# Optimization experiments

Hardware: AMD Instinct MI355X
Metric: run time of the kernel (lower is better)

The kernel has to match this reference:

```python
import jax, jax.numpy as jnp
import numpy as np

B, T, C, H = 4, 2048, 768, 12
D = C // H
EPS = 1e-5


def layernorm(x, g, b):
    mu = jnp.mean(x, axis=-1, keepdims=True)
    var = jnp.mean(jnp.square(x - mu), axis=-1, keepdims=True)
    return (x - mu) * jax.lax.rsqrt(var + EPS) * g + b


def setup_inputs() -> dict:
    key = jax.random.key(0)
    ks = jax.random.split(key, 16)
    s = 0.02
    return {
        "x": jax.random.normal(ks[0], (B, T, C), jnp.float32),
        "Wq": jax.random.normal(ks[1], (C, C), jnp.float32) * s,
        "bq": jnp.zeros((C,), jnp.float32),
        "Wk": jax.random.normal(ks[2], (C, C), jnp.float32) * s,
        "bk": jnp.zeros((C,), jnp.float32),
        "Wv": jax.random.normal(ks[3], (C, C), jnp.float32) * s,
        "bv": jnp.zeros((C,), jnp.float32),
        "Wo": jax.random.normal(ks[4], (C, C), jnp.float32) * s,
        "bo": jnp.zeros((C,), jnp.float32),
        "g1": jnp.ones((C,), jnp.float32),
        "b1": jnp.zeros((C,), jnp.float32),
        "g2": jnp.ones((C,), jnp.float32),
        "b2": jnp.zeros((C,), jnp.float32),
        "W1": jax.random.normal(ks[5], (C, 4 * C), jnp.float32) * s,
        "bm1": jnp.zeros((4 * C,), jnp.float32),
        "W2": jax.random.normal(ks[6], (4 * C, C), jnp.float32) * s,
        "bm2": jnp.zeros((C,), jnp.float32),
    }


def reference(x, Wq, bq, Wk, bk, Wv, bv, Wo, bo, g1, b1, g2, b2, W1, bm1, W2, bm2):
    # --- attention branch ---
    h = layernorm(x, g1, b1)
    q = (h @ Wq + bq).reshape(B, T, H, D)
    k = (h @ Wk + bk).reshape(B, T, H, D)
    v = (h @ Wv + bv).reshape(B, T, H, D)
    att = jnp.einsum('bqhd,bkhd->bhqk', q, k) / jnp.sqrt(jnp.float32(D))
    causal = jnp.tril(jnp.ones((T, T), bool))
    att = jnp.where(causal, att, -jnp.inf)
    att = jax.nn.softmax(att, axis=-1)
    o = jnp.einsum('bhqk,bkhd->bqhd', att, v).reshape(B, T, C)
    x = x + o @ Wo + bo
    # --- MLP branch ---
    h = layernorm(x, g2, b2)
    h = jax.nn.gelu(h @ W1 + bm1, approximate=False)
    return x + h @ W2 + bm2
```

## Files before the change

kernel.cpp:

```cpp
#include <hip/hip_runtime.h>
#include <hip/hip_bf16.h>

#define B_ 4
#define T_ 2048
#define C_ 768
#define H_ 12
#define D_ 64
#define QS_ 2304

typedef __attribute__((ext_vector_type(8))) short short8;
typedef __attribute__((ext_vector_type(4))) short short4v;
typedef __attribute__((ext_vector_type(4))) float f32x4;

__device__ __forceinline__ unsigned short f2bf(float f) {
    __hip_bfloat16 h = __float2bfloat16(f);
    return *reinterpret_cast<unsigned short*>(&h);
}

__device__ __forceinline__ unsigned cvt_pk_bf16(float lo, float hi) {
    unsigned r;
    asm("v_cvt_pk_bf16_f32 %0, %1, %2" : "=v"(r) : "v"(lo), "v"(hi));
    return r;
}

__device__ __forceinline__ void gl_lds16(const void* g, void* l) {
    __builtin_amdgcn_global_load_lds((const __attribute__((address_space(1))) unsigned int*)g,
                                     (__attribute__((address_space(3))) unsigned int*)l,
                                     16, 0, 0);
}

__global__ __launch_bounds__(256) void ln_f32_bf16(const float* __restrict__ x,
                                                   const float* __restrict__ g,
                                                   const float* __restrict__ b,
                                                   unsigned short* __restrict__ out) {
    int row = blockIdx.x;
    int tid = threadIdx.x;
    const float* xr = x + (size_t)row * C_;
    float v0 = xr[tid], v1 = xr[tid + 256], v2 = xr[tid + 512];
    float s = v0 + v1 + v2;
    #pragma unroll
    for (int off = 1; off < 64; off <<= 1) s += __shfl_xor(s, off);
    __shared__ float ws1[4], ws2[4];
    int wid = tid >> 6, lane = tid & 63;
    if (lane == 0) ws1[wid] = s;
    __syncthreads();
    float mean = (ws1[0] + ws1[1] + ws1[2] + ws1[3]) * (1.0f / C_);
    float d0 = v0 - mean, d1 = v1 - mean, d2 = v2 - mean;
    float qs = d0*d0 + d1*d1 + d2*d2;
    #pragma unroll
    for (int off = 1; off < 64; off <<= 1) qs += __shfl_xor(qs, off);
    if (lane == 0) ws2[wid] = qs;
    __syncthreads();
    float var = (ws2[0] + ws2[1] + ws2[2] + ws2[3]) * (1.0f / C_);
    float rs = rsqrtf(var + 1e-5f);
    unsigned short* orow = out + (size_t)row * C_;
    orow[tid]       = f2bf(d0 * rs * g[tid]       + b[tid]);
    orow[tid + 256] = f2bf(d1 * rs * g[tid + 256] + b[tid + 256]);
    orow[tid + 512] = f2bf(d2 * rs * g[tid + 512] + b[tid + 512]);
}

__global__ __launch_bounds__(256) void transpose_bf16(const float* __restrict__ W,
                                                      unsigned short* __restrict__ Wt,
                                                      int K, int N) {
    __shared__ float t[64][65];
    int n0 = blockIdx.x * 64, k0 = blockIdx.y * 64;
    int r = threadIdx.x >> 4, c4 = (threadIdx.x & 15) * 4;
    #pragma unroll
    for (int i = 0; i < 4; ++i) {
        float4 v = *(const float4*)(W + (size_t)(k0 + i * 16 + r) * N + n0 + c4);
        t[i*16 + r][c4 + 0] = v.x;
        t[i*16 + r][c4 + 1] = v.y;
        t[i*16 + r][c4 + 2] = v.z;
        t[i*16 + r][c4 + 3] = v.w;
    }
    __syncthreads();
    #pragma unroll
    for (int i = 0; i < 4; ++i) {
        ushort4 o;
        o.x = f2bf(t[c4 + 0][i*16 + r]);
        o.y = f2bf(t[c4 + 1][i*16 + r]);
        o.z = f2bf(t[c4 + 2][i*16 + r]);
        o.w = f2bf(t[c4 + 3][i*16 + r]);
        *(ushort4*)(Wt + (size_t)(n0 + i * 16 + r) * K + k0 + c4) = o;
    }
}

__global__ __launch_bounds__(256) void concat3(const float* __restrict__ a,
                                               const float* __restrict__ b,
                                               const float* __restrict__ c,
                                               float* __restrict__ o) {
    int i = blockIdx.x * 256 + threadIdx.x;
    o[i] = (i < 768) ? a[i] : (i < 1536) ? b[i - 768] : c[i - 1536];
}

template <int EPI>
__global__ __launch_bounds__(256) void gemm_bf16(const unsigned short* __restrict__ A,
                                                 const unsigned short* __restrict__ Bt,
                                                 const float* __restrict__ bias,
                                                 const float* __restrict__ resid,
                                                 void* __restrict__ Cout,
                                                 int M, int N, int K, int gx) {
    __shared__ short As[128 * 32];
    __shared__ short Bs[128 * 32];
    int tid = threadIdx.x;
    int w = tid >> 6, l = tid & 63;
    int nb = gridDim.x;
    int per = nb >> 3;
    int fid = (int)blockIdx.x;
    int wid = (fid & 7) * per + (fid >> 3);
    int bn = wid % gx, bm = wid / gx;
    int wr = w >> 1, wc = w & 1;

    f32x4 acc[4][4];
    #pragma unroll
    for (int m = 0; m < 4; ++m)
        #pragma unroll
        for (int n = 0; n < 4; ++n)
            acc[m][n] = (f32x4){0.f, 0.f, 0.f, 0.f};

    const short* Ag = (const short*)A + (size_t)(bm * 128) * K;
    const short* Bg = (const short*)Bt + (size_t)(bn * 128) * K;
    int srow = tid >> 2;
    int scol = (tid & 3) * 8;
    int lrow = l & 15, lk = (l >> 4) * 8;

    int nk = K / 32;
    for (int kt = 0; kt < nk; ++kt) {
        int k0 = kt * 32;
        if (kt > 0) __syncthreads();
        #pragma unroll
        for (int i = 0; i < 2; ++i) {
            gl_lds16(Ag + (size_t)(i * 64 + srow) * K + k0 + scol,
                     (char*)As + i * 4096 + w * 1024);
            gl_lds16(Bg + (size_t)(i * 64 + srow) * K + k0 + scol,
                     (char*)Bs + i * 4096 + w * 1024);
        }
        __syncthreads();

        short8 av[4], bv[4];
        #pragma unroll
        for (int m = 0; m < 4; ++m)
            av[m] = *(const short8*)&As[(wr * 64 + m * 16 + lrow) * 32 + lk];
        #pragma unroll
        for (int n = 0; n < 4; ++n)
            bv[n] = *(const short8*)&Bs[(wc * 64 + n * 16 + lrow) * 32 + lk];
        #pragma unroll
        for (int m = 0; m < 4; ++m)
            #pragma unroll
            for (int n = 0; n < 4; ++n)
                acc[m][n] = __builtin_amdgcn_mfma_f32_16x16x32_bf16(av[m], bv[n], acc[m][n], 0, 0, 0);
    }

    int lcol = l & 15, lr4 = (l >> 4) * 4;
    int row0 = bm * 128 + wr * 64;
    int col0 = bn * 128 + wc * 64;
    #pragma unroll
    for (int m = 0; m < 4; ++m) {
        #pragma unroll
        for (int n = 0; n < 4; ++n) {
            int col = col0 + n * 16 + lcol;
            float bz = bias[col];
            #pragma unroll
            for (int r = 0; r < 4; ++r) {
                int row = row0 + m * 16 + lr4 + r;
                float v = acc[m][n][r] + bz;
                if (EPI == 1) {
                    float u = fmaf(0.044715f * v, v * v, v);
                    float e = __builtin_amdgcn_exp2f(u * -2.3022127f);
                    v = v * __builtin_amdgcn_rcpf(1.0f + e);
                    ((unsigned short*)Cout)[(size_t)row * N + col] = f2bf(v);
                } else if (EPI == 2) {
                    v += resid[(size_t)row * N + col];
                    ((float*)Cout)[(size_t)row * N + col] = v;
                } else {
                    ((unsigned short*)Cout)[(size_t)row * N + col] = f2bf(v);
                }
            }
        }
    }
}

__global__ __launch_bounds__(256) void attn_mfma3(const unsigned short* __restrict__ QKV,
                                                  unsigned short* __restrict__ O) {
    __shared__ short Ks[128 * 64];
    __shared__ short Vt[64 * 128];

    int tid = threadIdx.x;
    int w = tid >> 6, l = tid & 63;
    int g = l >> 4, lc = l & 15;
    int wid = (int)(blockIdx.x & 7) * 96 + (int)(blockIdx.x >> 3);
    int bh = wid >> 4, pi = wid & 15;
    int b = bh / H_, h = bh % H_;
    const size_t bT = (size_t)b * T_;
    const unsigned short* Qp = QKV + h * D_;
    const unsigned short* Kp = QKV + 768 + h * D_;
    const unsigned short* Vp = QKV + 1536 + h * D_;
    const float SCL = 0.125f * 1.44269504088896340736f;

    for (int half = 0; half < 2; ++half) {
        int a = half ? pi : (31 - pi);
        int q0 = a * 64;
        int qw = q0 + w * 16;

        short8 qf[2];
        {
            const unsigned short* qp = Qp + (bT + qw + lc) * QS_;
            qf[0] = *(const short8*)(qp + g * 8);
            qf[1] = *(const short8*)(qp + 32 + g * 8);
        }

        f32x4 oacc[4];
        #pragma unroll
        for (int n = 0; n < 4; ++n) oacc[n] = (f32x4){0.f, 0.f, 0.f, 0.f};
        float mrun = 4.0f, lpart = 0.f;

        int ntiles = (a >> 1) + 1;
        for (int kt = 0; kt < ntiles; ++kt) {
            int k0 = kt * 128;
            if (half | kt) __syncthreads();
            #pragma unroll
            for (int c = 0; c < 4; ++c) {
                int row = w * 32 + c * 8 + (l >> 3);
                int inner = (l & 7) * 16;
                const char* src = (const char*)(Kp + (bT + k0 + row) * QS_)
                                  + (inner ^ ((row & 7) << 4));
                gl_lds16(src, (char*)Ks + w * 4096 + c * 1024);
            }
            #pragma unroll
            for (int dblk = 0; dblk < 4; ++dblk)
                #pragma unroll
                for (int pp = 0; pp < 2; ++pp) {
                    int d = lc + dblk * 16;
                    int kk0 = w * 32 + g * 4 + pp * 16;
                    const unsigned short* vp = Vp + (bT + k0 + kk0) * QS_ + d;
                    short4v pk = {(short)vp[0], (short)vp[QS_], (short)vp[2*QS_], (short)vp[3*QS_]};
                    int byt = (d * 256 + kk0 * 2) ^ ((d & 7) << 4);
                    *(short4v*)((char*)Vt + byt) = pk;
                }
            __syncthreads();

            uint2 qd[8];
            float lmax = -INFINITY;
            float rsum = 0.f;
            bool full = (k0 + 127 <= qw);
            #pragma unroll
            for (int mk = 0; mk < 8; ++mk) {
                f32x4 s = (f32x4){0.f, 0.f, 0.f, 0.f};
                __builtin_amdgcn_s_setprio(1);
                #pragma unroll
                for (int ksd = 0; ksd < 2; ++ksd) {
                    int row = mk * 16 + lc;
                    int byt = (row * 128 + ksd * 64 + g * 16) ^ ((row & 7) << 4);
                    short8 av = *(const short8*)((char*)Ks + byt);
                    s = __builtin_amdgcn_mfma_f32_16x16x32_bf16(av, qf[ksd], s, 0, 0, 0);
                }
                __builtin_amdgcn_s_setprio(0);
                float p[4];
                #pragma unroll
                for (int r = 0; r < 4; ++r) {
                    float sv = s[r] * SCL;
                    if (!full && (k0 + mk * 16 + g * 4 + r > qw + lc)) sv = -INFINITY;
                    lmax = fmaxf(lmax, sv);
                    float pv = __builtin_amdgcn_exp2f(sv - mrun);
                    p[r] = pv;
                    rsum += pv;
                }
                qd[mk].x = cvt_pk_bf16(p[0], p[1]);
                qd[mk].y = cvt_pk_bf16(p[2], p[3]);
            }
            lpart += rsum;

            #pragma unroll
            for (int ks = 0; ks < 4; ++ks) {
                uint2 qa = qd[ks * 2], qb = qd[ks * 2 + 1];
                int srcLo = lc + ((g & 1) << 5);
                int srcHi = srcLo + 16;
                unsigned a0 = (unsigned)__shfl((int)qa.x, srcLo);
                unsigned a1 = (unsigned)__shfl((int)qa.y, srcLo);
                unsigned a2 = (unsigned)__shfl((int)qa.x, srcHi);
                unsigned a3 = (unsigned)__shfl((int)qa.y, srcHi);
                unsigned b0 = (unsigned)__shfl((int)qb.x, srcLo);
                unsigned b1 = (unsigned)__shfl((int)qb.y, srcLo);
                unsigned b2 = (unsigned)__shfl((int)qb.x, srcHi);
                unsigned b3 = (unsigned)__shfl((int)qb.y, srcHi);
                bool lo = (g < 2);
                union { unsigned u[4]; short8 s8; } pa;
                pa.u[0] = lo ? a0 : b0;
                pa.u[1] = lo ? a1 : b1;
                pa.u[2] = lo ? a2 : b2;
                pa.u[3] = lo ? a3 : b3;
                short8 vbv[4];
                #pragma unroll
                for (int n = 0; n < 4; ++n) {
                    int row = n * 16 + lc;
                    int byt = (row * 256 + ks * 64 + g * 16) ^ ((row & 7) << 4);
                    vbv[n] = *(const short8*)((char*)Vt + byt);
                }
                __builtin_amdgcn_s_setprio(1);
                #pragma unroll
                for (int n = 0; n < 4; ++n)
                    oacc[n] = __builtin_amdgcn_mfma_f32_16x16x32_bf16(pa.s8, vbv[n], oacc[n], 0, 0, 0);
                __builtin_amdgcn_s_setprio(0);
            }

            if (__any(lmax > mrun + 8.0f)) {
                lmax = fmaxf(lmax, __shfl_xor(lmax, 16));
                lmax = fmaxf(lmax, __shfl_xor(lmax, 32));
                float mnew = fmaxf(mrun, lmax);
                float cc = __builtin_amdgcn_exp2f(mrun - mnew);
                lpart *= cc;
                mrun = mnew;
                #pragma unroll
                for (int r = 0; r < 4; ++r) {
                    float cr = __shfl(cc, (l & 48) + g * 4 + r);
                    #pragma unroll
                    for (int n = 0; n < 4; ++n) oacc[n][r] *= cr;
                }
            }
        }

        float lv = lpart;
        lv += __shfl_xor(lv, 16);
        lv += __shfl_xor(lv, 32);
        float linv = 1.0f / lv;
        float inv[4];
        #pragma unroll
        for (int r = 0; r < 4; ++r) inv[r] = __shfl(linv, (l & 48) + g * 4 + r);
        #pragma unroll
        for (int n = 0; n < 4; ++n) {
            int col = h * D_ + n * 16 + lc;
            #pragma unroll
            for (int r = 0; r < 4; ++r) {
                int row = qw + g * 4 + r;
                O[(bT + row) * C_ + col] = f2bf(oacc[n][r] * inv[r]);
            }
        }
    }
}

extern "C" void kernel_launch(void* const* d_in, const int* in_sizes, int n_in,
                              void* d_out, int out_size, void* d_ws, size_t ws_size,
                              hipStream_t stream) {
    const float* x   = (const float*)d_in[0];
    const float* Wq  = (const float*)d_in[1];
    const float* bq  = (const float*)d_in[2];
    const float* Wk  = (const float*)d_in[3];
    const float* bk  = (const float*)d_in[4];
    const float* Wv  = (const float*)d_in[5];
    const float* bv  = (const float*)d_in[6];
    const float* Wo  = (const float*)d_in[7];
    const float* bo  = (const float*)d_in[8];
    const float* g1  = (const float*)d_in[9];
    const float* b1  = (const float*)d_in[10];
    const float* g2  = (const float*)d_in[11];
    const float* b2  = (const float*)d_in[12];
    const float* W1  = (const float*)d_in[13];
    const float* bm1 = (const float*)d_in[14];
    const float* W2  = (const float*)d_in[15];
    const float* bm2 = (const float*)d_in[16];
    float* out = (float*)d_out;

    const size_t S = (size_t)B_ * T_ * C_;
    char* base = (char*)d_ws;
    unsigned short* ln1h = (unsigned short*)base;
    unsigned short* qkvb = (unsigned short*)(base + 2 * S);
    unsigned short* o    = ln1h;
    unsigned short* ln2h = qkvb;
    unsigned short* hid  = (unsigned short*)(base + 4 * S);
    float* xmid          = (float*)(base + 12 * S);
    unsigned short* wqkvt = (unsigned short*)(base + 16 * S);
    unsigned short* wot   = wqkvt + (size_t)3 * C_ * C_;
    unsigned short* w1t   = wot + (size_t)C_ * C_;
    unsigned short* w2t   = w1t + (size_t)C_ * 4 * C_;
    float* bqkv           = (float*)(w2t + (size_t)C_ * 4 * C_);

    const int M = B_ * T_;
    dim3 blk(256);

    transpose_bf16<<<dim3(C_ / 64, C_ / 64), blk, 0, stream>>>(Wq, wqkvt, C_, C_);
    transpose_bf16<<<dim3(C_ / 64, C_ / 64), blk, 0, stream>>>(Wk, wqkvt + (size_t)C_ * C_, C_, C_);
    transpose_bf16<<<dim3(C_ / 64, C_ / 64), blk, 0, stream>>>(Wv, wqkvt + (size_t)2 * C_ * C_, C_, C_);
    transpose_bf16<<<dim3(C_ / 64, C_ / 64), blk, 0, stream>>>(Wo, wot, C_, C_);
    transpose_bf16<<<dim3(4 * C_ / 64, C_ / 64), blk, 0, stream>>>(W1, w1t, C_, 4 * C_);
    transpose_bf16<<<dim3(C_ / 64, 4 * C_ / 64), blk, 0, stream>>>(W2, w2t, 4 * C_, C_);
    concat3<<<dim3(9), blk, 0, stream>>>(bq, bk, bv, bqkv);

    ln_f32_bf16<<<dim3(M), blk, 0, stream>>>(x, g1, b1, ln1h);

    gemm_bf16<3><<<dim3((QS_ / 128) * (M / 128)), blk, 0, stream>>>(ln1h, wqkvt, bqkv, nullptr, qkvb, M, QS_, C_, QS_ / 128);

    attn_mfma3<<<dim3(B_ * H_ * 16), blk, 0, stream>>>(qkvb, o);

    gemm_bf16<2><<<dim3((C_ / 128) * (M / 128)), blk, 0, stream>>>(o, wot, bo, x, xmid, M, C_, C_, C_ / 128);
    ln_f32_bf16<<<dim3(M), blk, 0, stream>>>(xmid, g2, b2, ln2h);
    gemm_bf16<1><<<dim3((4 * C_ / 128) * (M / 128)), blk, 0, stream>>>(ln2h, w1t, bm1, nullptr, hid, M, 4 * C_, C_, 4 * C_ / 128);
    gemm_bf16<2><<<dim3((C_ / 128) * (M / 128)), blk, 0, stream>>>(hid, w2t, bm2, xmid, out, M, C_, 4 * C_, C_ / 128);
}
```

Baseline: 356.0 us.

## Double-buffer GEMM and attention K/V tiles to overlap loads with MFMA

```diff
diff --git a/kernel.cpp b/kernel.cpp
--- a/kernel.cpp
+++ b/kernel.cpp
@@ -100,8 +100,8 @@
                                                  const float* __restrict__ resid,
                                                  void* __restrict__ Cout,
                                                  int M, int N, int K, int gx) {
-    __shared__ short As[128 * 32];
-    __shared__ short Bs[128 * 32];
+    __shared__ short As[2][128 * 32];
+    __shared__ short Bs[2][128 * 32];
     int tid = threadIdx.x;
     int w = tid >> 6, l = tid & 63;
     int nb = gridDim.x;
@@ -124,31 +124,38 @@
     int scol = (tid & 3) * 8;
     int lrow = l & 15, lk = (l >> 4) * 8;
 
-    int nk = K / 32;
-    for (int kt = 0; kt < nk; ++kt) {
-        int k0 = kt * 32;
-        if (kt > 0) __syncthreads();
+    auto stage = [&](int buf, int k0) {
         #pragma unroll
         for (int i = 0; i < 2; ++i) {
             gl_lds16(Ag + (size_t)(i * 64 + srow) * K + k0 + scol,
-                     (char*)As + i * 4096 + w * 1024);
+                     (char*)&As[buf][0] + i * 4096 + w * 1024);
             gl_lds16(Bg + (size_t)(i * 64 + srow) * K + k0 + scol,
-                     (char*)Bs + i * 4096 + w * 1024);
-        }
-        __syncthreads();
+                     (char*)&Bs[buf][0] + i * 4096 + w * 1024);
+        }
+    };
+
+    int nk = K / 32;
+    stage(0, 0);
+    __syncthreads();
+
+    for (int kt = 0; kt < nk; ++kt) {
+        int cur = kt & 1;
+        if (kt + 1 < nk) stage(cur ^ 1, (kt + 1) * 32);
 
         short8 av[4], bv[4];
         #pragma unroll
         for (int m = 0; m < 4; ++m)
-            av[m] = *(const short8*)&As[(wr * 64 + m * 16 + lrow) * 32 + lk];
+            av[m] = *(const short8*)&As[cur][(wr * 64 + m * 16 + lrow) * 32 + lk];
         #pragma unroll
         for (int n = 0; n < 4; ++n)
-            bv[n] = *(const short8*)&Bs[(wc * 64 + n * 16 + lrow) * 32 + lk];
+            bv[n] = *(const short8*)&Bs[cur][(wc * 64 + n * 16 + lrow) * 32 + lk];
         #pragma unroll
         for (int m = 0; m < 4; ++m)
             #pragma unroll
             for (int n = 0; n < 4; ++n)
                 acc[m][n] = __builtin_amdgcn_mfma_f32_16x16x32_bf16(av[m], bv[n], acc[m][n], 0, 0, 0);
+
+        __syncthreads();
     }
 
     int lcol = l & 15, lr4 = (l >> 4) * 4;
@@ -180,9 +187,9 @@
     }
 }
 
-__global__ __launch_bounds__(256) void attn_mfma3(const unsigned short* __restrict__ QKV,
-                                                  unsigned short* __restrict__ O) {
-    __shared__ short Ks[128 * 64];
+__global__ __launch_bounds__(256) void attn_v6(const unsigned short* __restrict__ QKV,
+                                               unsigned short* __restrict__ O) {
+    __shared__ short Ks[2 * 128 * 64];
     __shared__ short Vt[64 * 128];
 
     int tid = threadIdx.x;
@@ -196,11 +203,32 @@
     const unsigned short* Kp = QKV + 768 + h * D_;
     const unsigned short* Vp = QKV + 1536 + h * D_;
     const float SCL = 0.125f * 1.44269504088896340736f;
+    int vd = l;
+
+    short4v vreg[8];
+    auto loadV = [&](int K0) {
+        #pragma unroll
+        for (int pp = 0; pp < 8; ++pp) {
+            int kk0 = w * 32 + pp * 4;
+            const unsigned short* vp = Vp + (bT + K0 + kk0) * QS_ + vd;
+            vreg[pp] = (short4v){(short)vp[0], (short)vp[QS_],
+                                 (short)vp[2 * QS_], (short)vp[3 * QS_]};
+        }
+    };
+    auto stageK = [&](int K0, int buf) {
+        #pragma unroll
+        for (int c = 0; c < 4; ++c) {
+            int row = w * 32 + c * 8 + (l >> 3);
+            int inner = (l & 7) * 16;
+            const char* src = (const char*)(Kp + (bT + K0 + row) * QS_)
+                              + (inner ^ ((row & 7) << 4));
+            gl_lds16(src, (char*)Ks + buf * 16384 + w * 4096 + c * 1024);
+        }
+    };
 
     for (int half = 0; half < 2; ++half) {
         int a = half ? pi : (31 - pi);
-        int q0 = a * 64;
-        int qw = q0 + w * 16;
+        int qw = a * 64 + w * 16;
 
         short8 qf[2];
         {
@@ -215,29 +243,29 @@
         float mrun = 4.0f, lpart = 0.f;
 
         int ntiles = (a >> 1) + 1;
+
+        if (half) __syncthreads();
+        loadV(0);
+        stageK(0, 0);
+
         for (int kt = 0; kt < ntiles; ++kt) {
+            int cur = kt & 1;
             int k0 = kt * 128;
-            if (half | kt) __syncthreads();
-            #pragma unroll
-            for (int c = 0; c < 4; ++c) {
-                int row = w * 32 + c * 8 + (l >> 3);
-                int inner = (l & 7) * 16;
-                const char* src = (const char*)(Kp + (bT + k0 + row) * QS_)
-                                  + (inner ^ ((row & 7) << 4));
-                gl_lds16(src, (char*)Ks + w * 4096 + c * 1024);
-            }
-            #pragma unroll
-            for (int dblk = 0; dblk < 4; ++dblk)
-                #pragma unroll
-                for (int pp = 0; pp < 2; ++pp) {
-                    int d = lc + dblk * 16;
-                    int kk0 = w * 32 + g * 4 + pp * 16;
-                    const unsigned short* vp = Vp + (bT + k0 + kk0) * QS_ + d;
-                    short4v pk = {(short)vp[0], (short)vp[QS_], (short)vp[2*QS_], (short)vp[3*QS_]};
-                    int byt = (d * 256 + kk0 * 2) ^ ((d & 7) << 4);
-                    *(short4v*)((char*)Vt + byt) = pk;
-                }
+
             __syncthreads();
+
+            #pragma unroll
+            for (int pp = 0; pp < 8; ++pp) {
+                int kk0 = w * 32 + pp * 4;
+                int byt = (vd * 256 + kk0 * 2) ^ ((vd & 7) << 4);
+                *(short4v*)((char*)Vt + byt) = vreg[pp];
+            }
+            __syncthreads();
+
+            if (kt + 1 < ntiles) {
+                loadV((kt + 1) * 128);
+                stageK((kt + 1) * 128, cur ^ 1);
+            }
 
             uint2 qd[8];
             float lmax = -INFINITY;
@@ -251,7 +279,7 @@
                 for (int ksd = 0; ksd < 2; ++ksd) {
                     int row = mk * 16 + lc;
                     int byt = (row * 128 + ksd * 64 + g * 16) ^ ((row & 7) << 4);
-                    short8 av = *(const short8*)((char*)Ks + byt);
+                    short8 av = *(const short8*)((char*)Ks + cur * 16384 + byt);
                     s = __builtin_amdgcn_mfma_f32_16x16x32_bf16(av, qf[ksd], s, 0, 0, 0);
                 }
                 __builtin_amdgcn_s_setprio(0);
@@ -389,7 +417,7 @@
 
     gemm_bf16<3><<<dim3((QS_ / 128) * (M / 128)), blk, 0, stream>>>(ln1h, wqkvt, bqkv, nullptr, qkvb, M, QS_, C_, QS_ / 128);
 
-    attn_mfma3<<<dim3(B_ * H_ * 16), blk, 0, stream>>>(qkvb, o);
+    attn_v6<<<dim3(B_ * H_ * 16), blk, 0, stream>>>(qkvb, o);
 
     gemm_bf16<2><<<dim3((C_ / 128) * (M / 128)), blk, 0, stream>>>(o, wot, bo, x, xmid, M, C_, C_, C_ / 128);
     ln_f32_bf16<<<dim3(M), blk, 0, stream>>>(xmid, g2, b2, ln2h);
```

After: 339.6 us. 4.6% less time.

## Double-buffer GEMM LDS tiles and split attention into one query block per workgroup

Applied to the files above, without the earlier changes.

```diff
diff --git a/kernel.cpp b/kernel.cpp
--- a/kernel.cpp
+++ b/kernel.cpp
@@ -100,8 +100,8 @@
                                                  const float* __restrict__ resid,
                                                  void* __restrict__ Cout,
                                                  int M, int N, int K, int gx) {
-    __shared__ short As[128 * 32];
-    __shared__ short Bs[128 * 32];
+    __shared__ short As[2][128 * 32];
+    __shared__ short Bs[2][128 * 32];
     int tid = threadIdx.x;
     int w = tid >> 6, l = tid & 63;
     int nb = gridDim.x;
@@ -124,31 +124,38 @@
     int scol = (tid & 3) * 8;
     int lrow = l & 15, lk = (l >> 4) * 8;
 
-    int nk = K / 32;
-    for (int kt = 0; kt < nk; ++kt) {
-        int k0 = kt * 32;
-        if (kt > 0) __syncthreads();
+    auto stage = [&](int buf, int k0) {
         #pragma unroll
         for (int i = 0; i < 2; ++i) {
             gl_lds16(Ag + (size_t)(i * 64 + srow) * K + k0 + scol,
-                     (char*)As + i * 4096 + w * 1024);
+                     (char*)&As[buf][0] + i * 4096 + w * 1024);
             gl_lds16(Bg + (size_t)(i * 64 + srow) * K + k0 + scol,
-                     (char*)Bs + i * 4096 + w * 1024);
-        }
-        __syncthreads();
+                     (char*)&Bs[buf][0] + i * 4096 + w * 1024);
+        }
+    };
+
+    int nk = K / 32;
+    stage(0, 0);
+    __syncthreads();
+
+    for (int kt = 0; kt < nk; ++kt) {
+        int cur = kt & 1;
+        if (kt + 1 < nk) stage(cur ^ 1, (kt + 1) * 32);
 
         short8 av[4], bv[4];
         #pragma unroll
         for (int m = 0; m < 4; ++m)
-            av[m] = *(const short8*)&As[(wr * 64 + m * 16 + lrow) * 32 + lk];
+            av[m] = *(const short8*)&As[cur][(wr * 64 + m * 16 + lrow) * 32 + lk];
         #pragma unroll
         for (int n = 0; n < 4; ++n)
-            bv[n] = *(const short8*)&Bs[(wc * 64 + n * 16 + lrow) * 32 + lk];
+            bv[n] = *(const short8*)&Bs[cur][(wc * 64 + n * 16 + lrow) * 32 + lk];
         #pragma unroll
         for (int m = 0; m < 4; ++m)
             #pragma unroll
             for (int n = 0; n < 4; ++n)
                 acc[m][n] = __builtin_amdgcn_mfma_f32_16x16x32_bf16(av[m], bv[n], acc[m][n], 0, 0, 0);
+
+        __syncthreads();
     }
 
     int lcol = l & 15, lr4 = (l >> 4) * 4;
@@ -180,16 +187,17 @@
     }
 }
 
-__global__ __launch_bounds__(256) void attn_mfma3(const unsigned short* __restrict__ QKV,
-                                                  unsigned short* __restrict__ O) {
+__global__ __launch_bounds__(256) void attn_v7(const unsigned short* __restrict__ QKV,
+                                               unsigned short* __restrict__ O) {
     __shared__ short Ks[128 * 64];
     __shared__ short Vt[64 * 128];
 
     int tid = threadIdx.x;
     int w = tid >> 6, l = tid & 63;
     int g = l >> 4, lc = l & 15;
-    int wid = (int)(blockIdx.x & 7) * 96 + (int)(blockIdx.x >> 3);
-    int bh = wid >> 4, pi = wid & 15;
+    int wid = (int)(blockIdx.x & 7) * 192 + (int)(blockIdx.x >> 3);
+    int bh = wid >> 5;
+    int a  = 31 - (wid & 31);
     int b = bh / H_, h = bh % H_;
     const size_t bT = (size_t)b * T_;
     const unsigned short* Qp = QKV + h * D_;
@@ -197,143 +205,141 @@
     const unsigned short* Vp = QKV + 1536 + h * D_;
     const float SCL = 0.125f * 1.44269504088896340736f;
 
-    for (int half = 0; half < 2; ++half) {
-        int a = half ? pi : (31 - pi);
-        int q0 = a * 64;
-        int qw = q0 + w * 16;
-
-        short8 qf[2];
-        {
-            const unsigned short* qp = Qp + (bT + qw + lc) * QS_;
-            qf[0] = *(const short8*)(qp + g * 8);
-            qf[1] = *(const short8*)(qp + 32 + g * 8);
-        }
-
-        f32x4 oacc[4];
-        #pragma unroll
-        for (int n = 0; n < 4; ++n) oacc[n] = (f32x4){0.f, 0.f, 0.f, 0.f};
-        float mrun = 4.0f, lpart = 0.f;
-
-        int ntiles = (a >> 1) + 1;
-        for (int kt = 0; kt < ntiles; ++kt) {
-            int k0 = kt * 128;
-            if (half | kt) __syncthreads();
-            #pragma unroll
-            for (int c = 0; c < 4; ++c) {
-                int row = w * 32 + c * 8 + (l >> 3);
-                int inner = (l & 7) * 16;
-                const char* src = (const char*)(Kp + (bT + k0 + row) * QS_)
-                                  + (inner ^ ((row & 7) << 4));
-                gl_lds16(src, (char*)Ks + w * 4096 + c * 1024);
-            }
-            #pragma unroll
-            for (int dblk = 0; dblk < 4; ++dblk)
+    int qw = a * 64 + w * 16;
+
+    short8 qf[2];
+    {
+        const unsigned short* qp = Qp + (bT + qw + lc) * QS_;
+        qf[0] = *(const short8*)(qp + g * 8);
+        qf[1] = *(const short8*)(qp + 32 + g * 8);
+    }
+
+    f32x4 oacc[4];
+    #pragma unroll
+    for (int n = 0; n < 4; ++n) oacc[n] = (f32x4){0.f, 0.f, 0.f, 0.f};
+    float mrun = 4.0f, lpart = 0.f;
+
+    int ntiles = (a >> 1) + 1;
+    for (int kt = 0; kt < ntiles; ++kt) {
+        int k0 = kt * 128;
+        if (kt) __syncthreads();
+
+        #pragma unroll
+        for (int c = 0; c < 4; ++c) {
+            int row = w * 32 + c * 8 + (l >> 3);
+            int inner = (l & 7) * 16;
+            const char* src = (const char*)(Kp + (bT + k0 + row) * QS_)
+                              + (inner ^ ((row & 7) << 4));
+            gl_lds16(src, (char*)Ks + w * 4096 + c * 1024);
+        }
+        #pragma unroll
+        for (int dblk = 0; dblk < 4; ++dblk)
+            #pragma unroll
+            for (int pp = 0; pp < 2; ++pp) {
+                int d = lc + dblk * 16;
+                int kk0 = w * 32 + g * 4 + pp * 16;
+                const unsigned short* vp = Vp + (bT + k0 + kk0) * QS_ + d;
+                short4v pk = {(short)vp[0], (short)vp[QS_], (short)vp[2*QS_], (short)vp[3*QS_]};
+                int byt = (d * 256 + kk0 * 2) ^ ((d & 7) << 4);
+                *(short4v*)((char*)Vt + byt) = pk;
+            }
+        __syncthreads();
+
+        uint2 qd[8];
+        float lmaxP[4] = {-INFINITY, -INFINITY, -INFINITY, -INFINITY};
+        float rsumP[4] = {0.f, 0.f, 0.f, 0.f};
+        bool full = (k0 + 127 <= qw);
+        #pragma unroll
+        for (int mk = 0; mk < 8; ++mk) {
+            f32x4 s = (f32x4){0.f, 0.f, 0.f, 0.f};
+            __builtin_amdgcn_s_setprio(1);
+            #pragma unroll
+            for (int ksd = 0; ksd < 2; ++ksd) {
+                int row = mk * 16 + lc;
+                int byt = (row * 128 + ksd * 64 + g * 16) ^ ((row & 7) << 4);
+                short8 av = *(const short8*)((char*)Ks + byt);
+                s = __builtin_amdgcn_mfma_f32_16x16x32_bf16(av, qf[ksd], s, 0, 0, 0);
+            }
+            __builtin_amdgcn_s_setprio(0);
+            float p[4];
+            #pragma unroll
+            for (int r = 0; r < 4; ++r) {
+                float sv = s[r] * SCL;
+                if (!full && (k0 + mk * 16 + g * 4 + r > qw + lc)) sv = -INFINITY;
+                lmaxP[r] = fmaxf(lmaxP[r], sv);
+                float pv = __builtin_amdgcn_exp2f(sv - mrun);
+                p[r] = pv;
+                rsumP[r] += pv;
+            }
+            qd[mk].x = cvt_pk_bf16(p[0], p[1]);
+            qd[mk].y = cvt_pk_bf16(p[2], p[3]);
+        }
+        float lmax = fmaxf(fmaxf(lmaxP[0], lmaxP[1]), fmaxf(lmaxP[2], lmaxP[3]));
+        lpart += (rsumP[0] + rsumP[1]) + (rsumP[2] + rsumP[3]);
+
+        #pragma unroll
+        for (int ks = 0; ks < 4; ++ks) {
+            uint2 qa = qd[ks * 2], qb = qd[ks * 2 + 1];
+            int srcLo = lc + ((g & 1) << 5);
+            int srcHi = srcLo + 16;
+            unsigned a0 = (unsigned)__shfl((int)qa.x, srcLo);
+            unsigned a1 = (unsigned)__shfl((int)qa.y, srcLo);
+            unsigned a2 = (unsigned)__shfl((int)qa.x, srcHi);
+            unsigned a3 = (unsigned)__shfl((int)qa.y, srcHi);
+            unsigned b0 = (unsigned)__shfl((int)qb.x, srcLo);
+            unsigned b1 = (unsigned)__shfl((int)qb.y, srcLo);
+            unsigned b2 = (unsigned)__shfl((int)qb.x, srcHi);
+            unsigned b3 = (unsigned)__shfl((int)qb.y, srcHi);
+            bool lo = (g < 2);
+            union { unsigned u[4]; short8 s8; } pa;
+            pa.u[0] = lo ? a0 : b0;
+            pa.u[1] = lo ? a1 : b1;
+            pa.u[2] = lo ? a2 : b2;
+            pa.u[3] = lo ? a3 : b3;
+            short8 vbv[4];
+            #pragma unroll
+            for (int n = 0; n < 4; ++n) {
+                int row = n * 16 + lc;
+                int byt = (row * 256 + ks * 64 + g * 16) ^ ((row & 7) << 4);
+                vbv[n] = *(const short8*)((char*)Vt + byt);
+            }
+            __builtin_amdgcn_s_setprio(1);
+            #pragma unroll
+            for (int n = 0; n < 4; ++n)
+                oacc[n] = __builtin_amdgcn_mfma_f32_16x16x32_bf16(pa.s8, vbv[n], oacc[n], 0, 0, 0);
+            __builtin_amdgcn_s_setprio(0);
+        }
+
+        if (__any(lmax > mrun + 8.0f)) {
+            lmax = fmaxf(lmax, __shfl_xor(lmax, 16));
+            lmax = fmaxf(lmax, __shfl_xor(lmax, 32));
+            float mnew = fmaxf(mrun, lmax);
+            float cc = __builtin_amdgcn_exp2f(mrun - mnew);
+            lpart *= cc;
+            mrun = mnew;
+            #pragma unroll
+            for (int r = 0; r < 4; ++r) {
+                float cr = __shfl(cc, (l & 48) + g * 4 + r);
                 #pragma unroll
-                for (int pp = 0; pp < 2; ++pp) {
-                    int d = lc + dblk * 16;
-                    int kk0 = w * 32 + g * 4 + pp * 16;
-                    const unsigned short* vp = Vp + (bT + k0 + kk0) * QS_ + d;
-                    short4v pk = {(short)vp[0], (short)vp[QS_], (short)vp[2*QS_], (short)vp[3*QS_]};
-                    int byt = (d * 256 + kk0 * 2) ^ ((d & 7) << 4);
-                    *(short4v*)((char*)Vt + byt) = pk;
-                }
-            __syncthreads();
-
-            uint2 qd[8];
-            float lmax = -INFINITY;
-            float rsum = 0.f;
-            bool full = (k0 + 127 <= qw);
-            #pragma unroll
-            for (int mk = 0; mk < 8; ++mk) {
-                f32x4 s = (f32x4){0.f, 0.f, 0.f, 0.f};
-                __builtin_amdgcn_s_setprio(1);
-                #pragma unroll
-                for (int ksd = 0; ksd < 2; ++ksd) {
-                    int row = mk * 16 + lc;
-                    int byt = (row * 128 + ksd * 64 + g * 16) ^ ((row & 7) << 4);
-                    short8 av = *(const short8*)((char*)Ks + byt);
-                    s = __builtin_amdgcn_mfma_f32_16x16x32_bf16(av, qf[ksd], s, 0, 0, 0);
-                }
-                __builtin_amdgcn_s_setprio(0);
-                float p[4];
-                #pragma unroll
-                for (int r = 0; r < 4; ++r) {
-                    float sv = s[r] * SCL;
-                    if (!full && (k0 + mk * 16 + g * 4 + r > qw + lc)) sv = -INFINITY;
-                    lmax = fmaxf(lmax, sv);
-                    float pv = __builtin_amdgcn_exp2f(sv - mrun);
-                    p[r] = pv;
-                    rsum += pv;
-                }
-                qd[mk].x = cvt_pk_bf16(p[0], p[1]);
-                qd[mk].y = cvt_pk_bf16(p[2], p[3]);
-            }
-            lpart += rsum;
-
-            #pragma unroll
-            for (int ks = 0; ks < 4; ++ks) {
-                uint2 qa = qd[ks * 2], qb = qd[ks * 2 + 1];
-                int srcLo = lc + ((g & 1) << 5);
-                int srcHi = srcLo + 16;
-                unsigned a0 = (unsigned)__shfl((int)qa.x, srcLo);
-                unsigned a1 = (unsigned)__shfl((int)qa.y, srcLo);
-                unsigned a2 = (unsigned)__shfl((int)qa.x, srcHi);
-                unsigned a3 = (unsigned)__shfl((int)qa.y, srcHi);
-                unsigned b0 = (unsigned)__shfl((int)qb.x, srcLo);
-                unsigned b1 = (unsigned)__shfl((int)qb.y, srcLo);
-                unsigned b2 = (unsigned)__shfl((int)qb.x, srcHi);
-                unsigned b3 = (unsigned)__shfl((int)qb.y, srcHi);
-                bool lo = (g < 2);
-                union { unsigned u[4]; short8 s8; } pa;
-                pa.u[0] = lo ? a0 : b0;
-                pa.u[1] = lo ? a1 : b1;
-                pa.u[2] = lo ? a2 : b2;
-                pa.u[3] = lo ? a3 : b3;
-                short8 vbv[4];
-                #pragma unroll
-                for (int n = 0; n < 4; ++n) {
-                    int row = n * 16 + lc;
-                    int byt = (row * 256 + ks * 64 + g * 16) ^ ((row & 7) << 4);
-                    vbv[n] = *(const short8*)((char*)Vt + byt);
-                }
-                __builtin_amdgcn_s_setprio(1);
-                #pragma unroll
-                for (int n = 0; n < 4; ++n)
-                    oacc[n] = __builtin_amdgcn_mfma_f32_16x16x32_bf16(pa.s8, vbv[n], oacc[n], 0, 0, 0);
-                __builtin_amdgcn_s_setprio(0);
-            }
-
-            if (__any(lmax > mrun + 8.0f)) {
-                lmax = fmaxf(lmax, __shfl_xor(lmax, 16));
-                lmax = fmaxf(lmax, __shfl_xor(lmax, 32));
-                float mnew = fmaxf(mrun, lmax);
-                float cc = __builtin_amdgcn_exp2f(mrun - mnew);
-                lpart *= cc;
-                mrun = mnew;
-                #pragma unroll
-                for (int r = 0; r < 4; ++r) {
-                    float cr = __shfl(cc, (l & 48) + g * 4 + r);
-                    #pragma unroll
-                    for (int n = 0; n < 4; ++n) oacc[n][r] *= cr;
-                }
-            }
-        }
-
-        float lv = lpart;
-        lv += __shfl_xor(lv, 16);
-        lv += __shfl_xor(lv, 32);
-        float linv = 1.0f / lv;
-        float inv[4];
-        #pragma unroll
-        for (int r = 0; r < 4; ++r) inv[r] = __shfl(linv, (l & 48) + g * 4 + r);
-        #pragma unroll
-        for (int n = 0; n < 4; ++n) {
-            int col = h * D_ + n * 16 + lc;
-            #pragma unroll
-            for (int r = 0; r < 4; ++r) {
-                int row = qw + g * 4 + r;
-                O[(bT + row) * C_ + col] = f2bf(oacc[n][r] * inv[r]);
-            }
+                for (int n = 0; n < 4; ++n) oacc[n][r] *= cr;
+            }
+        }
+    }
+
+    float lv = lpart;
+    lv += __shfl_xor(lv, 16);
+    lv += __shfl_xor(lv, 32);
+    float linv = 1.0f / lv;
+    float inv[4];
+    #pragma unroll
+    for (int r = 0; r < 4; ++r) inv[r] = __shfl(linv, (l & 48) + g * 4 + r);
+    #pragma unroll
+    for (int n = 0; n < 4; ++n) {
+        int col = h * D_ + n * 16 + lc;
+        #pragma unroll
+        for (int r = 0; r < 4; ++r) {
+            int row = qw + g * 4 + r;
+            O[(bT + row) * C_ + col] = f2bf(oacc[n][r] * inv[r]);
         }
     }
 }
@@ -389,7 +395,7 @@
 
     gemm_bf16<3><<<dim3((QS_ / 128) * (M / 128)), blk, 0, stream>>>(ln1h, wqkvt, bqkv, nullptr, qkvb, M, QS_, C_, QS_ / 128);
 
-    attn_mfma3<<<dim3(B_ * H_ * 16), blk, 0, stream>>>(qkvb, o);
+    attn_v7<<<dim3(B_ * H_ * 32), blk, 0, stream>>>(qkvb, o);
 
     gemm_bf16<2><<<dim3((C_ / 128) * (M / 128)), blk, 0, stream>>>(o, wot, bo, x, xmid, M, C_, C_, C_ / 128);
     ln_f32_bf16<<<dim3(M), blk, 0, stream>>>(xmid, g2, b2, ln2h);
```

Measured after the change: 321.5 us. 9.7% less time.
